# Performance work log

Measured on AMD Instinct MI355X. Metric: run time of the kernel, lower is better.

Reference implementation:

```python
import jax, jax.numpy as jnp
import numpy as np

B, L, D = 32, 1024, 256
H, DH = 4, 128  # dim_per_head = model_dim//num_heads*2

def setup_inputs() -> dict:
    key = jax.random.key(0)
    ks = jax.random.split(key, 8)
    initrange = 0.02
    return {
        "key":   jax.random.normal(ks[0], (B, L, D), jnp.float32),
        "value": jax.random.normal(ks[1], (B, L, D), jnp.float32),
        "query": jax.random.normal(ks[2], (B, L, D), jnp.float32),
        "Wq": jax.random.normal(ks[3], (H * DH, D), jnp.float32) * initrange,
        "bq": jnp.zeros((H * DH,), jnp.float32),
        "Wk": jax.random.normal(ks[4], (H * DH, D), jnp.float32) * initrange,
        "bk": jnp.zeros((H * DH,), jnp.float32),
        "Wv": jax.random.normal(ks[5], (H * DH, D), jnp.float32) * initrange,
        "bv": jnp.zeros((H * DH,), jnp.float32),
        "Wf": jax.random.normal(ks[6], (D, 2 * D), jnp.float32) * initrange,
        "bf": jnp.zeros((D,), jnp.float32),
    }

def reference(key, value, query, Wq, bq, Wk, bk, Wv, bv, Wf, bf):
    b, l, d = query.shape
    # QKV projections: [B,L,D] -> [B,L,H*DH] -> [B,H,L,DH]
    def proj(x, W, bias):
        return (x @ W.T + bias).reshape(b, -1, H, DH).transpose(0, 2, 1, 3)
    q = proj(query, Wq, bq)
    k = proj(key, Wk, bk)
    v = proj(value, Wv, bv)
    # NOTE: source computes q*scale but discards it (overwritten), so NO scaling.
    attn = jnp.einsum('bhqd,bhkd->bhqk', q, k)  # [B,H,L,L]
    attn = jax.nn.softmax(attn, axis=-1)        # dropout is identity in eval
    ctx = jnp.einsum('bhqk,bhkd->bhqd', attn, v)
    ctx = ctx.transpose(0, 2, 1, 3).reshape(b, -1, H * DH)  # [B,L,2*D]
    out = ctx @ Wf.T + bf                        # [B,L,D]
    return out, attn
```

## Files before the change

### kernel.cpp

```cpp
#include <hip/hip_runtime.h>
#include <hip/hip_bf16.h>
#include <stdint.h>


#define B_  32
#define L_  1024
#define D_  256
#define H_  4
#define DH_ 128

typedef __attribute__((ext_vector_type(8))) short bf16x8;
typedef __attribute__((ext_vector_type(4))) float f32x4;

#define MFMA16(a, b, c) __builtin_amdgcn_mfma_f32_16x16x32_bf16((a), (b), (c), 0, 0, 0)

__device__ __forceinline__ uint16_t f2bf(float x) {
  uint32_t u = __float_as_uint(x);
  u += 0x7FFFu + ((u >> 16) & 1u);
  return (uint16_t)(u >> 16);
}
__device__ __forceinline__ float bf2f(uint16_t h) {
  return __uint_as_float((uint32_t)h << 16);
}

__global__ __launch_bounds__(256) void proj_kernel(
    const float* __restrict__ Xq, const float* __restrict__ Xk, const float* __restrict__ Xv,
    const float* __restrict__ Wq, const float* __restrict__ bq,
    const float* __restrict__ Wk, const float* __restrict__ bk,
    const float* __restrict__ Wv, const float* __restrict__ bv,
    uint16_t* __restrict__ Qh, uint16_t* __restrict__ Ql,
    uint16_t* __restrict__ Kh, uint16_t* __restrict__ Kl,
    uint16_t* __restrict__ Vt)
{
  const int mode = blockIdx.z;
  const float* X    = (mode == 0) ? Xq : (mode == 1) ? Xk : Xv;
  const float* W    = (mode == 0) ? Wq : (mode == 1) ? Wk : Wv;
  const float* bias = (mode == 0) ? bq : (mode == 1) ? bk : bv;

  __shared__ __align__(16) uint8_t smem[65536];
  uint8_t* XhS = smem;
  uint8_t* XlS = smem + 16384;
  uint8_t* WhS = smem + 32768;
  uint8_t* WlS = smem + 49152;

  const int t  = threadIdx.x;
  const int m0 = blockIdx.x * 64;
  const int n0 = blockIdx.y * 64;
  const int w = t >> 6, l = t & 63, lg = l >> 4, l16 = l & 15;
  const int wm = (w >> 1) * 32, wn = (w & 1) * 32;

  f32x4 acc[2][2] = {};

  for (int kc = 0; kc < 2; ++kc) {
    __syncthreads();
    #pragma unroll
    for (int i = 0; i < 8; ++i) {
      int f = i * 256 + t;
      int row = f >> 5, c4 = f & 31;
      f32x4 v = *reinterpret_cast<const f32x4*>(X + (size_t)(m0 + row) * 256 + kc * 128 + c4 * 4);
      uint32_t byte = (((uint32_t)row * 256 + (uint32_t)c4 * 8)) ^ ((uint32_t)(row & 7) << 4);
      uint16_t h0 = f2bf(v[0]), h1 = f2bf(v[1]), h2 = f2bf(v[2]), h3 = f2bf(v[3]);
      *reinterpret_cast<uint2*>(XhS + byte) =
          make_uint2((uint32_t)h0 | ((uint32_t)h1 << 16), (uint32_t)h2 | ((uint32_t)h3 << 16));
      if (mode < 2) {
        uint16_t e0 = f2bf(v[0] - bf2f(h0)), e1 = f2bf(v[1] - bf2f(h1));
        uint16_t e2 = f2bf(v[2] - bf2f(h2)), e3 = f2bf(v[3] - bf2f(h3));
        *reinterpret_cast<uint2*>(XlS + byte) =
            make_uint2((uint32_t)e0 | ((uint32_t)e1 << 16), (uint32_t)e2 | ((uint32_t)e3 << 16));
      }
    }
    #pragma unroll
    for (int i = 0; i < 8; ++i) {
      int f = i * 256 + t;
      int row = f >> 5, c4 = f & 31;
      f32x4 v = *reinterpret_cast<const f32x4*>(W + (size_t)(n0 + row) * 256 + kc * 128 + c4 * 4);
      uint32_t byte = (((uint32_t)row * 256 + (uint32_t)c4 * 8)) ^ ((uint32_t)(row & 7) << 4);
      uint16_t h0 = f2bf(v[0]), h1 = f2bf(v[1]), h2 = f2bf(v[2]), h3 = f2bf(v[3]);
      *reinterpret_cast<uint2*>(WhS + byte) =
          make_uint2((uint32_t)h0 | ((uint32_t)h1 << 16), (uint32_t)h2 | ((uint32_t)h3 << 16));
      if (mode < 2) {
        uint16_t e0 = f2bf(v[0] - bf2f(h0)), e1 = f2bf(v[1] - bf2f(h1));
        uint16_t e2 = f2bf(v[2] - bf2f(h2)), e3 = f2bf(v[3] - bf2f(h3));
        *reinterpret_cast<uint2*>(WlS + byte) =
            make_uint2((uint32_t)e0 | ((uint32_t)e1 << 16), (uint32_t)e2 | ((uint32_t)e3 << 16));
      }
    }
    __syncthreads();

    #pragma unroll
    for (int ks = 0; ks < 4; ++ks) {
      bf16x8 ah[2], al[2], bh[2], bl[2];
      #pragma unroll
      for (int mt = 0; mt < 2; ++mt) {
        int row = wm + mt * 16 + l16;
        uint32_t byte = ((uint32_t)row * 256 + (uint32_t)(ks * 64 + lg * 16)) ^ ((uint32_t)(row & 7) << 4);
        ah[mt] = *reinterpret_cast<bf16x8*>(XhS + byte);
        if (mode < 2) al[mt] = *reinterpret_cast<bf16x8*>(XlS + byte);
      }
      #pragma unroll
      for (int nt = 0; nt < 2; ++nt) {
        int row = wn + nt * 16 + l16;
        uint32_t byte = ((uint32_t)row * 256 + (uint32_t)(ks * 64 + lg * 16)) ^ ((uint32_t)(row & 7) << 4);
        bh[nt] = *reinterpret_cast<bf16x8*>(WhS + byte);
        if (mode < 2) bl[nt] = *reinterpret_cast<bf16x8*>(WlS + byte);
      }
      #pragma unroll
      for (int mt = 0; mt < 2; ++mt)
        #pragma unroll
        for (int nt = 0; nt < 2; ++nt) {
          acc[mt][nt] = MFMA16(ah[mt], bh[nt], acc[mt][nt]);
          if (mode < 2) {
            acc[mt][nt] = MFMA16(ah[mt], bl[nt], acc[mt][nt]);
            acc[mt][nt] = MFMA16(al[mt], bh[nt], acc[mt][nt]);
          }
        }
    }
  }

  #pragma unroll
  for (int nt = 0; nt < 2; ++nt) {
    int n = n0 + wn + nt * 16 + l16;
    float bias_v = bias[n];
    int hh = n >> 7, d = n & 127;
    #pragma unroll
    for (int mt = 0; mt < 2; ++mt) {
      #pragma unroll
      for (int r = 0; r < 4; ++r) {
        int m = m0 + wm + mt * 16 + lg * 4 + r;
        int bb = m >> 10, lq = m & 1023;
        float val = acc[mt][nt][r] + bias_v;
        if (mode == 2) {
          Vt[((size_t)(bb * 4 + hh) * 128 + d) * 1024 + lq] = f2bf(val);
        } else {
          size_t idx = ((size_t)(bb * 4 + hh) * 1024 + lq) * 128 + d;
          uint16_t hv = f2bf(val);
          uint16_t lv = f2bf(val - bf2f(hv));
          if (mode == 0) { Qh[idx] = hv; Ql[idx] = lv; }
          else           { Kh[idx] = hv; Kl[idx] = lv; }
        }
      }
    }
  }
}

__global__ __launch_bounds__(512) void attn_kernel(
    const uint16_t* __restrict__ Qhg, const uint16_t* __restrict__ Qlg,
    const uint16_t* __restrict__ Khg, const uint16_t* __restrict__ Klg,
    const uint16_t* __restrict__ Vtg, uint16_t* __restrict__ ctx,
    float* __restrict__ attn_out)
{
  __shared__ __align__(16) uint8_t pbuf[65536];

  const int bid = blockIdx.x;
  const int swz = (bid & 7) * 512 + (bid >> 3);
  const int b = swz >> 7, h = (swz >> 5) & 3, q0 = (swz & 31) * 32;

  const int t = threadIdx.x;
  const int w = t >> 6, l = t & 63, lg = l >> 4, l16 = l & 15;

  const size_t bh = (size_t)(b * 4 + h);
  const uint16_t* Qhp = Qhg + bh * (size_t)(L_ * DH_);
  const uint16_t* Qlp = Qlg + bh * (size_t)(L_ * DH_);
  const uint16_t* Khp = Khg + bh * (size_t)(L_ * DH_);
  const uint16_t* Klp = Klg + bh * (size_t)(L_ * DH_);
  const uint16_t* Vp  = Vtg + bh * (size_t)(DH_ * L_);

  bf16x8 qfh[2][4], qfl[2][4];
  #pragma unroll
  for (int qt = 0; qt < 2; ++qt)
    #pragma unroll
    for (int ds = 0; ds < 4; ++ds) {
      size_t off = (size_t)(q0 + qt * 16 + l16) * 128 + ds * 32 + lg * 8;
      qfh[qt][ds] = *reinterpret_cast<const bf16x8*>(Qhp + off);
      qfl[qt][ds] = *reinterpret_cast<const bf16x8*>(Qlp + off);
    }

  f32x4 acc[2][8] = {};
  #pragma unroll
  for (int kt = 0; kt < 8; ++kt) {
    #pragma unroll
    for (int ds = 0; ds < 4; ++ds) {
      size_t off = (size_t)(w * 128 + kt * 16 + l16) * 128 + ds * 32 + lg * 8;
      bf16x8 kfh = *reinterpret_cast<const bf16x8*>(Khp + off);
      bf16x8 kfl = *reinterpret_cast<const bf16x8*>(Klp + off);
      #pragma unroll
      for (int qt = 0; qt < 2; ++qt) {
        acc[qt][kt] = MFMA16(kfh, qfh[qt][ds], acc[qt][kt]);
        acc[qt][kt] = MFMA16(kfh, qfl[qt][ds], acc[qt][kt]);
        acc[qt][kt] = MFMA16(kfl, qfh[qt][ds], acc[qt][kt]);
      }
    }
  }

  float part[2] = {0.f, 0.f};
  #pragma unroll
  for (int qt = 0; qt < 2; ++qt)
    #pragma unroll
    for (int kt = 0; kt < 8; ++kt)
      #pragma unroll
      for (int r = 0; r < 4; ++r) {
        float e = __expf(acc[qt][kt][r]);
        acc[qt][kt][r] = e;
        part[qt] += e;
      }
  #pragma unroll
  for (int qt = 0; qt < 2; ++qt) {
    part[qt] += __shfl_xor(part[qt], 16, 64);
    part[qt] += __shfl_xor(part[qt], 32, 64);
  }
  {
    float* sums = reinterpret_cast<float*>(pbuf);
    if (l < 16) { sums[w * 32 + l16] = part[0]; sums[w * 32 + 16 + l16] = part[1]; }
  }
  __syncthreads();
  float inv[2];
  {
    const float* sums = reinterpret_cast<const float*>(pbuf);
    #pragma unroll
    for (int qt = 0; qt < 2; ++qt) {
      float s = 0.f;
      #pragma unroll
      for (int ww = 0; ww < 8; ++ww) s += sums[ww * 32 + qt * 16 + l16];
      inv[qt] = 1.0f / s;
    }
  }
  __syncthreads();

  float* attn_bh = attn_out + bh * (size_t)(L_ * L_);
  #pragma unroll
  for (int qt = 0; qt < 2; ++qt) {
    int q = q0 + qt * 16 + l16;
    #pragma unroll
    for (int kt = 0; kt < 8; ++kt) {
      f32x4 o = acc[qt][kt] * inv[qt];
      int kcol = w * 128 + kt * 16 + lg * 4;
      *reinterpret_cast<f32x4*>(attn_bh + (size_t)q * 1024 + kcol) = o;
      int qr = qt * 16 + l16;
      uint32_t byte = ((uint32_t)w * 8192 + (uint32_t)qr * 256 + (uint32_t)(kt * 16 + lg * 4) * 2)
                      ^ ((uint32_t)(qr & 7) << 4);
      uint32_t lo = (uint32_t)f2bf(o[0]) | ((uint32_t)f2bf(o[1]) << 16);
      uint32_t hi = (uint32_t)f2bf(o[2]) | ((uint32_t)f2bf(o[3]) << 16);
      *reinterpret_cast<uint2*>(pbuf + byte) = make_uint2(lo, hi);
    }
  }

  f32x4 cacc[2][8] = {};
  #pragma unroll
  for (int kc = 0; kc < 4; ++kc) {
    bf16x8 pa[2];
    #pragma unroll
    for (int qt = 0; qt < 2; ++qt) {
      int qr = qt * 16 + l16;
      uint32_t byte = ((uint32_t)w * 8192 + (uint32_t)qr * 256 + (uint32_t)(kc * 32 + lg * 8) * 2)
                      ^ ((uint32_t)(qr & 7) << 4);
      pa[qt] = *reinterpret_cast<bf16x8*>(pbuf + byte);
    }
    #pragma unroll
    for (int dt = 0; dt < 8; ++dt) {
      bf16x8 vb = *reinterpret_cast<const bf16x8*>(
          Vp + (size_t)(dt * 16 + l16) * 1024 + w * 128 + kc * 32 + lg * 8);
      cacc[0][dt] = MFMA16(pa[0], vb, cacc[0][dt]);
      cacc[1][dt] = MFMA16(pa[1], vb, cacc[1][dt]);
    }
  }

  __syncthreads();
  if (w < 4) {
    uint8_t* buf = pbuf + w * 16384;
    #pragma unroll
    for (int qt = 0; qt < 2; ++qt)
      #pragma unroll
      for (int dt = 0; dt < 8; ++dt) {
        int d = dt * 16 + l16, q = qt * 16 + lg * 4;
        uint32_t byte = ((uint32_t)(d * 32 + q) * 4) ^ ((uint32_t)(d & 7) << 4);
        *reinterpret_cast<f32x4*>(buf + byte) = cacc[qt][dt];
      }
  }
  __syncthreads();
  if (w >= 4) {
    uint8_t* buf = pbuf + (w - 4) * 16384;
    #pragma unroll
    for (int qt = 0; qt < 2; ++qt)
      #pragma unroll
      for (int dt = 0; dt < 8; ++dt) {
        int d = dt * 16 + l16, q = qt * 16 + lg * 4;
        uint32_t byte = ((uint32_t)(d * 32 + q) * 4) ^ ((uint32_t)(d & 7) << 4);
        f32x4 x = *reinterpret_cast<f32x4*>(buf + byte);
        x += cacc[qt][dt];
        *reinterpret_cast<f32x4*>(buf + byte) = x;
      }
  }
  __syncthreads();
  {
    uint32_t off = (uint32_t)(t & 255) * 64;
    uint8_t* dst = pbuf + ((t < 256) ? 0u : 16384u) + off;
    const uint8_t* src = dst + 32768;
    #pragma unroll
    for (int j = 0; j < 4; ++j) {
      f32x4 x = *reinterpret_cast<f32x4*>(dst + j * 16);
      f32x4 y = *reinterpret_cast<const f32x4*>(src + j * 16);
      x += y;
      *reinterpret_cast<f32x4*>(dst + j * 16) = x;
    }
  }
  __syncthreads();
  {
    uint32_t off = (uint32_t)t * 32;
    uint8_t* dst = pbuf + off;
    const uint8_t* src = pbuf + 16384 + off;
    #pragma unroll
    for (int j = 0; j < 2; ++j) {
      f32x4 x = *reinterpret_cast<f32x4*>(dst + j * 16);
      f32x4 y = *reinterpret_cast<const f32x4*>(src + j * 16);
      x += y;
      *reinterpret_cast<f32x4*>(dst + j * 16) = x;
    }
  }
  __syncthreads();
  {
    int q = t >> 4;
    int dc = (t & 15) * 8;
    bf16x8 sv;
    #pragma unroll
    for (int j = 0; j < 8; ++j) {
      int d = dc + j;
      uint32_t byte = ((uint32_t)(d * 32 + q) * 4) ^ ((uint32_t)(d & 7) << 4);
      sv[j] = (short)f2bf(*reinterpret_cast<float*>(pbuf + byte));
    }
    size_t row = (size_t)b * 1024 + (size_t)(q0 + q);
    *reinterpret_cast<bf16x8*>(ctx + row * 512 + h * 128 + dc) = sv;
  }
}

__global__ __launch_bounds__(256) void outproj_kernel(
    const uint16_t* __restrict__ ctx, const float* __restrict__ Wf,
    const float* __restrict__ bfp, float* __restrict__ out)
{
  __shared__ __align__(16) uint8_t smem[65536];
  uint8_t* Cs = smem;
  uint8_t* Ws = smem + 32768;

  const int t = threadIdx.x;
  const int m0 = blockIdx.x * 64, n0 = blockIdx.y * 64;
  const int w = t >> 6, l = t & 63, lg = l >> 4, l16 = l & 15;
  const int wm = (w >> 1) * 32, wn = (w & 1) * 32;

  f32x4 acc[2][2] = {};

  for (int kc = 0; kc < 2; ++kc) {
    __syncthreads();
    #pragma unroll
    for (int i = 0; i < 8; ++i) {
      int f = i * 256 + t;
      int row = f >> 5, c16 = f & 31;
      bf16x8 v = *reinterpret_cast<const bf16x8*>(ctx + (size_t)(m0 + row) * 512 + kc * 256 + c16 * 8);
      uint32_t byte = ((uint32_t)row * 512 + (uint32_t)c16 * 16) ^ ((uint32_t)(row & 7) << 4);
      *reinterpret_cast<bf16x8*>(Cs + byte) = v;
    }
    #pragma unroll
    for (int i = 0; i < 16; ++i) {
      int f = i * 256 + t;
      int row = f >> 6, c4 = f & 63;
      f32x4 v = *reinterpret_cast<const f32x4*>(Wf + (size_t)(n0 + row) * 512 + kc * 256 + c4 * 4);
      uint32_t byte = ((uint32_t)row * 512 + (uint32_t)c4 * 8) ^ ((uint32_t)(row & 7) << 4);
      uint16_t h0 = f2bf(v[0]), h1 = f2bf(v[1]), h2 = f2bf(v[2]), h3 = f2bf(v[3]);
      *reinterpret_cast<uint2*>(Ws + byte) =
          make_uint2((uint32_t)h0 | ((uint32_t)h1 << 16), (uint32_t)h2 | ((uint32_t)h3 << 16));
    }
    __syncthreads();

    #pragma unroll
    for (int ks = 0; ks < 8; ++ks) {
      bf16x8 a[2], bb[2];
      #pragma unroll
      for (int mt = 0; mt < 2; ++mt) {
        int row = wm + mt * 16 + l16;
        uint32_t byte = ((uint32_t)row * 512 + (uint32_t)(ks * 64 + lg * 16)) ^ ((uint32_t)(row & 7) << 4);
        a[mt] = *reinterpret_cast<bf16x8*>(Cs + byte);
      }
      #pragma unroll
      for (int nt = 0; nt < 2; ++nt) {
        int row = wn + nt * 16 + l16;
        uint32_t byte = ((uint32_t)row * 512 + (uint32_t)(ks * 64 + lg * 16)) ^ ((uint32_t)(row & 7) << 4);
        bb[nt] = *reinterpret_cast<bf16x8*>(Ws + byte);
      }
      #pragma unroll
      for (int mt = 0; mt < 2; ++mt)
        #pragma unroll
        for (int nt = 0; nt < 2; ++nt)
          acc[mt][nt] = MFMA16(a[mt], bb[nt], acc[mt][nt]);
    }
  }

  #pragma unroll
  for (int nt = 0; nt < 2; ++nt) {
    int n = n0 + wn + nt * 16 + l16;
    float bias_v = bfp[n];
    #pragma unroll
    for (int mt = 0; mt < 2; ++mt)
      #pragma unroll
      for (int r = 0; r < 4; ++r) {
        int m = m0 + wm + mt * 16 + lg * 4 + r;
        out[(size_t)m * 256 + n] = acc[mt][nt][r] + bias_v;
      }
  }
}

extern "C" void kernel_launch(void* const* d_in, const int* in_sizes, int n_in,
                              void* d_out, int out_size, void* d_ws, size_t ws_size,
                              hipStream_t stream) {
  const float* key   = (const float*)d_in[0];
  const float* value = (const float*)d_in[1];
  const float* query = (const float*)d_in[2];
  const float* Wq = (const float*)d_in[3];
  const float* bq = (const float*)d_in[4];
  const float* Wk = (const float*)d_in[5];
  const float* bk = (const float*)d_in[6];
  const float* Wv = (const float*)d_in[7];
  const float* bv = (const float*)d_in[8];
  const float* Wf = (const float*)d_in[9];
  const float* bf = (const float*)d_in[10];

  float* out  = (float*)d_out;
  float* attn = out + (size_t)B_ * L_ * D_;

  const size_t TSZ = (size_t)B_ * H_ * L_ * DH_;
  uint16_t* Qh  = (uint16_t*)d_ws;
  uint16_t* Ql  = Qh + TSZ;
  uint16_t* Kh  = Ql + TSZ;
  uint16_t* Kl  = Kh + TSZ;
  uint16_t* Vt  = Kl + TSZ;
  uint16_t* ctx = Vt + TSZ;

  proj_kernel<<<dim3(512, 8, 3), 256, 0, stream>>>(
      query, key, value, Wq, bq, Wk, bk, Wv, bv, Qh, Ql, Kh, Kl, Vt);
  attn_kernel<<<dim3(4096), 512, 0, stream>>>(Qh, Ql, Kh, Kl, Vt, ctx, attn);
  outproj_kernel<<<dim3(512, 4), 256, 0, stream>>>(ctx, Wf, bf, out);
}
```

Baseline: 1.826 ms.

## Restructure attention into per-wave row tiles with two-pass softmax

Each wave now owns 16 query rows and walks all 1024 keys. A first pass uses only the hi part of Q to get the softmax row sum, and a second pass recomputes the scores in split precision, normalizes them, streams attn with nontemporal stores and feeds P·V straight from a small per-wave LDS scratch. This removes the 64KB shared buffer, the cross-wave sum exchange and the multi-stage cross-wave reduction of ctx, which lowers LDS use and raises occupancy. In exchange it recomputes QK^T, and the row sum comes from the hi-only scores, so the normalization differs slightly from the split-precision numerator. K is also reloaded by each wave, which raises L2 traffic.

```diff
diff --git a/kernel.cpp b/kernel.cpp
--- a/kernel.cpp
+++ b/kernel.cpp
@@ -21,6 +21,9 @@
 }
 __device__ __forceinline__ float bf2f(uint16_t h) {
   return __uint_as_float((uint32_t)h << 16);
+}
+__device__ __forceinline__ uint32_t pk2(float a, float b) {
+  return (uint32_t)f2bf(a) | ((uint32_t)f2bf(b) << 16);
 }
 
 __global__ __launch_bounds__(256) void proj_kernel(
@@ -143,20 +146,21 @@
   }
 }
 
-__global__ __launch_bounds__(512) void attn_kernel(
+__global__ __launch_bounds__(256, 4) void attn_kernel(
     const uint16_t* __restrict__ Qhg, const uint16_t* __restrict__ Qlg,
     const uint16_t* __restrict__ Khg, const uint16_t* __restrict__ Klg,
     const uint16_t* __restrict__ Vtg, uint16_t* __restrict__ ctx,
     float* __restrict__ attn_out)
 {
-  __shared__ __align__(16) uint8_t pbuf[65536];
+  __shared__ __align__(16) uint8_t scratch[4 * 1280];
 
   const int bid = blockIdx.x;
-  const int swz = (bid & 7) * 512 + (bid >> 3);
-  const int b = swz >> 7, h = (swz >> 5) & 3, q0 = (swz & 31) * 32;
+  const int swz = (bid & 7) * 256 + (bid >> 3);
+  const int b = swz >> 6, h = (swz >> 4) & 3, q0 = (swz & 15) * 64;
 
   const int t = threadIdx.x;
   const int w = t >> 6, l = t & 63, lg = l >> 4, l16 = l & 15;
+  const int qw = q0 + w * 16;
 
   const size_t bh = (size_t)(b * 4 + h);
   const uint16_t* Qhp = Qhg + bh * (size_t)(L_ * DH_);
@@ -164,171 +168,78 @@
   const uint16_t* Khp = Khg + bh * (size_t)(L_ * DH_);
   const uint16_t* Klp = Klg + bh * (size_t)(L_ * DH_);
   const uint16_t* Vp  = Vtg + bh * (size_t)(DH_ * L_);
-
-  bf16x8 qfh[2][4], qfl[2][4];
-  #pragma unroll
-  for (int qt = 0; qt < 2; ++qt)
-    #pragma unroll
-    for (int ds = 0; ds < 4; ++ds) {
-      size_t off = (size_t)(q0 + qt * 16 + l16) * 128 + ds * 32 + lg * 8;
-      qfh[qt][ds] = *reinterpret_cast<const bf16x8*>(Qhp + off);
-      qfl[qt][ds] = *reinterpret_cast<const bf16x8*>(Qlp + off);
-    }
-
-  f32x4 acc[2][8] = {};
-  #pragma unroll
-  for (int kt = 0; kt < 8; ++kt) {
-    #pragma unroll
-    for (int ds = 0; ds < 4; ++ds) {
-      size_t off = (size_t)(w * 128 + kt * 16 + l16) * 128 + ds * 32 + lg * 8;
-      bf16x8 kfh = *reinterpret_cast<const bf16x8*>(Khp + off);
-      bf16x8 kfl = *reinterpret_cast<const bf16x8*>(Klp + off);
-      #pragma unroll
-      for (int qt = 0; qt < 2; ++qt) {
-        acc[qt][kt] = MFMA16(kfh, qfh[qt][ds], acc[qt][kt]);
-        acc[qt][kt] = MFMA16(kfh, qfl[qt][ds], acc[qt][kt]);
-        acc[qt][kt] = MFMA16(kfl, qfh[qt][ds], acc[qt][kt]);
-      }
-    }
-  }
-
-  float part[2] = {0.f, 0.f};
-  #pragma unroll
-  for (int qt = 0; qt < 2; ++qt)
-    #pragma unroll
-    for (int kt = 0; kt < 8; ++kt)
-      #pragma unroll
-      for (int r = 0; r < 4; ++r) {
-        float e = __expf(acc[qt][kt][r]);
-        acc[qt][kt][r] = e;
-        part[qt] += e;
-      }
-  #pragma unroll
-  for (int qt = 0; qt < 2; ++qt) {
-    part[qt] += __shfl_xor(part[qt], 16, 64);
-    part[qt] += __shfl_xor(part[qt], 32, 64);
-  }
-  {
-    float* sums = reinterpret_cast<float*>(pbuf);
-    if (l < 16) { sums[w * 32 + l16] = part[0]; sums[w * 32 + 16 + l16] = part[1]; }
-  }
-  __syncthreads();
-  float inv[2];
-  {
-    const float* sums = reinterpret_cast<const float*>(pbuf);
-    #pragma unroll
-    for (int qt = 0; qt < 2; ++qt) {
-      float s = 0.f;
-      #pragma unroll
-      for (int ww = 0; ww < 8; ++ww) s += sums[ww * 32 + qt * 16 + l16];
-      inv[qt] = 1.0f / s;
-    }
-  }
-  __syncthreads();
-
-  float* attn_bh = attn_out + bh * (size_t)(L_ * L_);
-  #pragma unroll
-  for (int qt = 0; qt < 2; ++qt) {
-    int q = q0 + qt * 16 + l16;
-    #pragma unroll
-    for (int kt = 0; kt < 8; ++kt) {
-      f32x4 o = acc[qt][kt] * inv[qt];
-      int kcol = w * 128 + kt * 16 + lg * 4;
-      *reinterpret_cast<f32x4*>(attn_bh + (size_t)q * 1024 + kcol) = o;
-      int qr = qt * 16 + l16;
-      uint32_t byte = ((uint32_t)w * 8192 + (uint32_t)qr * 256 + (uint32_t)(kt * 16 + lg * 4) * 2)
-                      ^ ((uint32_t)(qr & 7) << 4);
-      uint32_t lo = (uint32_t)f2bf(o[0]) | ((uint32_t)f2bf(o[1]) << 16);
-      uint32_t hi = (uint32_t)f2bf(o[2]) | ((uint32_t)f2bf(o[3]) << 16);
-      *reinterpret_cast<uint2*>(pbuf + byte) = make_uint2(lo, hi);
-    }
-  }
-
-  f32x4 cacc[2][8] = {};
-  #pragma unroll
-  for (int kc = 0; kc < 4; ++kc) {
-    bf16x8 pa[2];
-    #pragma unroll
-    for (int qt = 0; qt < 2; ++qt) {
-      int qr = qt * 16 + l16;
-      uint32_t byte = ((uint32_t)w * 8192 + (uint32_t)qr * 256 + (uint32_t)(kc * 32 + lg * 8) * 2)
-                      ^ ((uint32_t)(qr & 7) << 4);
-      pa[qt] = *reinterpret_cast<bf16x8*>(pbuf + byte);
-    }
+  uint8_t* sp = scratch + w * 1280;
+
+  bf16x8 qfh[4];
+  #pragma unroll
+  for (int ds = 0; ds < 4; ++ds)
+    qfh[ds] = *reinterpret_cast<const bf16x8*>(Qhp + (size_t)(qw + l16) * 128 + ds * 32 + lg * 8);
+
+  float sum = 0.f;
+  #pragma unroll 2
+  for (int kt = 0; kt < 64; ++kt) {
+    bf16x8 kf[4];
+    #pragma unroll
+    for (int ds = 0; ds < 4; ++ds)
+      kf[ds] = *reinterpret_cast<const bf16x8*>(Khp + (size_t)(kt * 16 + l16) * 128 + ds * 32 + lg * 8);
+    f32x4 a = {};
+    #pragma unroll
+    for (int ds = 0; ds < 4; ++ds) a = MFMA16(kf[ds], qfh[ds], a);
+    sum += __expf(a[0]) + __expf(a[1]) + __expf(a[2]) + __expf(a[3]);
+  }
+  sum += __shfl_xor(sum, 16, 64);
+  sum += __shfl_xor(sum, 32, 64);
+  const float inv = 1.0f / sum;
+
+  bf16x8 qfl[4];
+  #pragma unroll
+  for (int ds = 0; ds < 4; ++ds)
+    qfl[ds] = *reinterpret_cast<const bf16x8*>(Qlp + (size_t)(qw + l16) * 128 + ds * 32 + lg * 8);
+
+  f32x4 cacc[8] = {};
+  float* attn_q = attn_out + bh * (size_t)(L_ * L_) + (size_t)(qw + l16) * 1024;
+
+  for (int kp = 0; kp < 32; ++kp) {
+    #pragma unroll
+    for (int h2 = 0; h2 < 2; ++h2) {
+      const int kt = kp * 2 + h2;
+      bf16x8 kfh[4], kfl[4];
+      #pragma unroll
+      for (int ds = 0; ds < 4; ++ds) {
+        size_t off = (size_t)(kt * 16 + l16) * 128 + ds * 32 + lg * 8;
+        kfh[ds] = *reinterpret_cast<const bf16x8*>(Khp + off);
+        kfl[ds] = *reinterpret_cast<const bf16x8*>(Klp + off);
+      }
+      f32x4 a = {};
+      #pragma unroll
+      for (int ds = 0; ds < 4; ++ds) {
+        a = MFMA16(kfh[ds], qfh[ds], a);
+        a = MFMA16(kfh[ds], qfl[ds], a);
+        a = MFMA16(kfl[ds], qfh[ds], a);
+      }
+      f32x4 e;
+      #pragma unroll
+      for (int r = 0; r < 4; ++r) e[r] = __expf(a[r]) * inv;
+      __builtin_nontemporal_store(e, reinterpret_cast<f32x4*>(attn_q + kt * 16 + lg * 4));
+      *reinterpret_cast<uint2*>(sp + l16 * 80 + h2 * 32 + lg * 8) =
+          make_uint2(pk2(e[0], e[1]), pk2(e[2], e[3]));
+    }
+    bf16x8 pa = *reinterpret_cast<bf16x8*>(sp + l16 * 80 + lg * 16);
     #pragma unroll
     for (int dt = 0; dt < 8; ++dt) {
       bf16x8 vb = *reinterpret_cast<const bf16x8*>(
-          Vp + (size_t)(dt * 16 + l16) * 1024 + w * 128 + kc * 32 + lg * 8);
-      cacc[0][dt] = MFMA16(pa[0], vb, cacc[0][dt]);
-      cacc[1][dt] = MFMA16(pa[1], vb, cacc[1][dt]);
-    }
-  }
-
-  __syncthreads();
-  if (w < 4) {
-    uint8_t* buf = pbuf + w * 16384;
-    #pragma unroll
-    for (int qt = 0; qt < 2; ++qt)
-      #pragma unroll
-      for (int dt = 0; dt < 8; ++dt) {
-        int d = dt * 16 + l16, q = qt * 16 + lg * 4;
-        uint32_t byte = ((uint32_t)(d * 32 + q) * 4) ^ ((uint32_t)(d & 7) << 4);
-        *reinterpret_cast<f32x4*>(buf + byte) = cacc[qt][dt];
-      }
-  }
-  __syncthreads();
-  if (w >= 4) {
-    uint8_t* buf = pbuf + (w - 4) * 16384;
-    #pragma unroll
-    for (int qt = 0; qt < 2; ++qt)
-      #pragma unroll
-      for (int dt = 0; dt < 8; ++dt) {
-        int d = dt * 16 + l16, q = qt * 16 + lg * 4;
-        uint32_t byte = ((uint32_t)(d * 32 + q) * 4) ^ ((uint32_t)(d & 7) << 4);
-        f32x4 x = *reinterpret_cast<f32x4*>(buf + byte);
-        x += cacc[qt][dt];
-        *reinterpret_cast<f32x4*>(buf + byte) = x;
-      }
-  }
-  __syncthreads();
-  {
-    uint32_t off = (uint32_t)(t & 255) * 64;
-    uint8_t* dst = pbuf + ((t < 256) ? 0u : 16384u) + off;
-    const uint8_t* src = dst + 32768;
-    #pragma unroll
-    for (int j = 0; j < 4; ++j) {
-      f32x4 x = *reinterpret_cast<f32x4*>(dst + j * 16);
-      f32x4 y = *reinterpret_cast<const f32x4*>(src + j * 16);
-      x += y;
-      *reinterpret_cast<f32x4*>(dst + j * 16) = x;
-    }
-  }
-  __syncthreads();
-  {
-    uint32_t off = (uint32_t)t * 32;
-    uint8_t* dst = pbuf + off;
-    const uint8_t* src = pbuf + 16384 + off;
-    #pragma unroll
-    for (int j = 0; j < 2; ++j) {
-      f32x4 x = *reinterpret_cast<f32x4*>(dst + j * 16);
-      f32x4 y = *reinterpret_cast<const f32x4*>(src + j * 16);
-      x += y;
-      *reinterpret_cast<f32x4*>(dst + j * 16) = x;
-    }
-  }
-  __syncthreads();
-  {
-    int q = t >> 4;
-    int dc = (t & 15) * 8;
-    bf16x8 sv;
-    #pragma unroll
-    for (int j = 0; j < 8; ++j) {
-      int d = dc + j;
-      uint32_t byte = ((uint32_t)(d * 32 + q) * 4) ^ ((uint32_t)(d & 7) << 4);
-      sv[j] = (short)f2bf(*reinterpret_cast<float*>(pbuf + byte));
-    }
-    size_t row = (size_t)b * 1024 + (size_t)(q0 + q);
-    *reinterpret_cast<bf16x8*>(ctx + row * 512 + h * 128 + dc) = sv;
+          Vp + (size_t)(dt * 16 + l16) * 1024 + kp * 32 + lg * 8);
+      cacc[dt] = MFMA16(pa, vb, cacc[dt]);
+    }
+  }
+
+  #pragma unroll
+  for (int dt = 0; dt < 8; ++dt) {
+    #pragma unroll
+    for (int r = 0; r < 4; ++r) {
+      size_t row = (size_t)b * 1024 + (size_t)(qw + lg * 4 + r);
+      ctx[row * 512 + h * 128 + dt * 16 + l16] = f2bf(cacc[dt][r]);
+    }
   }
 }
 
@@ -434,6 +345,6 @@
 
   proj_kernel<<<dim3(512, 8, 3), 256, 0, stream>>>(
       query, key, value, Wq, bq, Wk, bk, Wv, bv, Qh, Ql, Kh, Kl, Vt);
-  attn_kernel<<<dim3(4096), 512, 0, stream>>>(Qh, Ql, Kh, Kl, Vt, ctx, attn);
+  attn_kernel<<<dim3(2048), 256, 0, stream>>>(Qh, Ql, Kh, Kl, Vt, ctx, attn);
   outproj_kernel<<<dim3(512, 4), 256, 0, stream>>>(ctx, Wf, bf, out);
 }
```

Result: slower. 1.992 ms (+9.1%).
